# Kernel optimization log

Hardware: AMD Instinct MI355X
Metric: run time of the kernel (lower is better)

## Reference

```python
import jax, jax.numpy as jnp
import numpy as np

HS = 256      # hidden_size
HD = 256      # hidden_dim
B, L, S = 256, 400, 512
N = B * L
E = N * 4
NEG_SLOPE = 0.2


def setup_inputs() -> dict:
    key = jax.random.key(0)
    ks = iter(jax.random.split(key, 48))
    def rn(shape, scale=0.05):
        return jax.random.normal(next(ks), shape, jnp.float32) * scale
    inp = {}
    inp['emb'] = jax.random.normal(next(ks), (N, 640), jnp.float32)
    inp['x_tokens'] = jax.random.randint(next(ks), (N,), 0, 6, jnp.int32)
    inp['edge_src'] = jax.random.randint(next(ks), (E,), 0, N, jnp.int32)
    inp['edge_dst'] = jax.random.randint(next(ks), (E,), 0, N, jnp.int32)
    inp['batch_ids'] = (jnp.arange(N, dtype=jnp.int32) // L)
    inp['pos_ids'] = (jnp.arange(N, dtype=jnp.int32) % L)
    inp['mask'] = (jnp.arange(S)[None, :] < L).astype(jnp.float32) * jnp.ones((B, 1), jnp.float32)
    # parameters
    inp['emb_table'] = rn((6, HS))
    inp['W_e2g'] = rn((640, HS)); inp['b_e2g'] = jnp.zeros((HS,), jnp.float32)
    # GAT layers: (in, heads*out), att_src/att_dst [heads, out], bias [out]
    inp['W1'] = rn((HS, 4 * HD)); inp['asrc1'] = rn((4, HD)); inp['adst1'] = rn((4, HD)); inp['b1'] = jnp.zeros((HD,), jnp.float32)
    inp['W2'] = rn((HD, 4 * HD)); inp['asrc2'] = rn((4, HD)); inp['adst2'] = rn((4, HD)); inp['b2'] = jnp.zeros((HD,), jnp.float32)
    inp['W3'] = rn((HD, 1 * HS)); inp['asrc3'] = rn((1, HS)); inp['adst3'] = rn((1, HS)); inp['b3'] = jnp.zeros((HS,), jnp.float32)
    inp['W_le'] = rn((640, HS)); inp['b_le'] = jnp.zeros((HS,), jnp.float32)
    # CNN conv kernels: OIH layout [out=128, in=256, k]
    inp['k7'] = rn((HS // 2, HS, 7)); inp['cb7'] = jnp.zeros((HS // 2,), jnp.float32)
    inp['k11'] = rn((HS // 2, HS, 11)); inp['cb11'] = jnp.zeros((HS // 2,), jnp.float32)
    inp['k15'] = rn((HS // 2, HS, 15)); inp['cb15'] = jnp.zeros((HS // 2,), jnp.float32)
    inp['Wl1'] = rn((HS // 2, 512)); inp['bl1'] = jnp.zeros((512,), jnp.float32)
    inp['Wl2'] = rn((512, HS)); inp['bl2'] = jnp.zeros((HS,), jnp.float32)
    return inp


def _gat(x, src, dst, W, a_src, a_dst, b, heads, out_dim):
    # PyG GATConv, concat=False, eval (no dropout), with self-loops.
    n = x.shape[0]
    h = (x @ W).reshape(n, heads, out_dim)             # [N,H,C]
    al_s = (h * a_src[None]).sum(-1)                   # [N,H]
    al_d = (h * a_dst[None]).sum(-1)                   # [N,H]
    e = al_s[src] + al_d[dst]                          # [E,H]
    e = jnp.where(e > 0, e, NEG_SLOPE * e)             # leaky_relu(0.2)
    m = jax.ops.segment_max(e, dst, num_segments=n)
    m = jnp.where(jnp.isfinite(m), m, 0.0)
    ex = jnp.exp(e - m[dst])
    denom = jax.ops.segment_sum(ex, dst, num_segments=n) + 1e-16
    alpha = ex / denom[dst]                            # [E,H]
    out = jax.ops.segment_sum(alpha[:, :, None] * h[src], dst, num_segments=n)
    return out.mean(axis=1) + b                        # concat=False -> mean over heads


def _conv1d(x, w, b, pad):
    # x: [B,C,S], w: [O,I,k]
    y = jax.lax.conv_general_dilated(x, w, (1,), [(pad, pad)],
                                     dimension_numbers=('NCH', 'OIH', 'NCH'))
    return y + b[None, :, None]


def reference(emb, x_tokens, edge_src, edge_dst, batch_ids, pos_ids, mask,
              emb_table, W_e2g, b_e2g,
              W1, asrc1, adst1, b1, W2, asrc2, adst2, b2, W3, asrc3, adst3, b3,
              W_le, b_le, k7, cb7, k11, cb11, k15, cb15, Wl1, bl1, Wl2, bl2):
    n = emb.shape[0]
    # self-loops (PyG GATConv default)
    loops = jnp.arange(n, dtype=edge_src.dtype)
    src = jnp.concatenate([edge_src, loops])
    dst = jnp.concatenate([edge_dst, loops])

    x_r = emb_table[x_tokens]                          # [N,HS]
    x_g = jax.nn.relu(emb @ W_e2g + b_e2g)             # [N,HS]
    x = jax.nn.relu(_gat(x_g, src, dst, W1, asrc1, adst1, b1, 4, HD))
    x = jax.nn.relu(_gat(x, src, dst, W2, asrc2, adst2, b2, 4, HD))
    x = jax.nn.relu(_gat(x, src, dst, W3, asrc3, adst3, b3, 1, HS))

    emb_l = jax.nn.relu(emb @ W_le + b_le)             # [N,HS]

    # ragged -> padded [B,S,HS] via scatter (vectorized form of the python loop)
    zeros = jnp.zeros((mask.shape[0], S, HS), jnp.float32)
    out_r = zeros.at[batch_ids, pos_ids].set((x_r + emb_l) / 2)

    # CNN (eval: dropout = identity)
    xc = out_r.transpose(0, 2, 1)                      # [B,HS,S]
    x1 = _conv1d(xc, k7, cb7, 3)
    x2 = _conv1d(xc, k11, cb11, 5)
    x3 = _conv1d(xc, k15, cb15, 7)
    xc = ((x1 + x2 + x3) / 3).transpose(0, 2, 1)       # [B,S,128]
    xc = jax.nn.relu(xc @ Wl1 + bl1) @ Wl2 + bl2       # [B,S,HS]

    emb_seq = (xc * mask[:, :, None]).mean(axis=1)     # [B,HS]
    return emb_seq
```

## Files before the change

kernel.cpp:

```cpp
#include <hip/hip_runtime.h>

#define NNODES 102400
#define NBATCH 256
#define LSEQ   400
#define SPAD   416
#define HS     256
#define KDIM   640
#define OC     128
#define NTAP   15
#define H1     512
#define STILE  80
#define SROWS  94

typedef __attribute__((ext_vector_type(8))) short short8;
typedef __attribute__((ext_vector_type(4))) float floatx4;

__device__ inline unsigned short f2bf(float f) {
    unsigned u = __builtin_bit_cast(unsigned, f);
    unsigned r = (u + 0x7FFFu + ((u >> 16) & 1u)) >> 16;
    return (unsigned short)r;
}

__device__ inline void gld_lds16(const void* g, void* l) {
    __builtin_amdgcn_global_load_lds(
        (const __attribute__((address_space(1))) unsigned int*)g,
        (__attribute__((address_space(3))) unsigned int*)l, 16, 0, 0);
}

__global__ __launch_bounds__(256) void setup_all(
    const float* __restrict__ k7, const float* __restrict__ k11,
    const float* __restrict__ k15, const float* __restrict__ cb7,
    const float* __restrict__ cb11, const float* __restrict__ cb15,
    const float* __restrict__ W_le, const float* __restrict__ Wl1,
    unsigned short* __restrict__ Wpk, float* __restrict__ bc,
    unsigned short* __restrict__ Wle_pk, unsigned short* __restrict__ Wl1_pk,
    unsigned short* __restrict__ seq, float* __restrict__ A_acc)
{
    int bid = blockIdx.x, tid = threadIdx.x;
    if (bid < 512) {
        int idx = bid * 256 + tid;
        int b = idx >> 9, within = idx & 511;
        int rowi = within >> 5, c = within & 31;
        int srow = rowi < 8 ? rowi : 400 + rowi;
        ((uint4*)seq)[((size_t)b * SPAD + srow) * 32 + c] = make_uint4(0u, 0u, 0u, 0u);
    } else if (bid < 2432) {
        int idx = (bid - 512) * 256 + tid;
        int oc = idx & (OC - 1);
        int ic = (idx >> 7) & (HS - 1);
        int d  = idx / (OC * HS);
        float wv = k15[(oc * HS + ic) * 15 + d];
        int t11 = d - 2;
        if (t11 >= 0 && t11 < 11) wv += k11[(oc * HS + ic) * 11 + t11];
        int t7 = d - 4;
        if (t7 >= 0 && t7 < 7)   wv += k7[(oc * HS + ic) * 7 + t7];
        wv *= (1.0f / 3.0f);
        int kc = ic >> 6, ks = (ic >> 5) & 1, qq = (ic >> 3) & 3, j = ic & 7;
        int nt = oc >> 4, n = oc & 15;
        int pidx = ((((d * 4 + kc) * 2 + ks) * 8 + nt) * 64 + (qq * 16 + n)) * 8 + j;
        Wpk[pidx] = f2bf(wv);
        if (idx < OC) bc[idx] = (cb7[idx] + cb11[idx] + cb15[idx]) * (1.0f / 3.0f);
    } else if (bid < 3072) {
        int idx = (bid - 2432) * 256 + tid;
        int k = idx >> 8, col = idx & 255;
        int t = k >> 6, ks = (k >> 5) & 1, qq = (k >> 3) & 3, j = k & 7;
        int nt = col >> 4, n = col & 15;
        int pidx = (((t * 2 + ks) * 16 + nt) * 64 + (qq * 16 + n)) * 8 + j;
        Wle_pk[pidx] = f2bf(W_le[k * 256 + col]);
    } else if (bid < 3328) {
        int idx = (bid - 3072) * 256 + tid;
        int k = idx >> 9, col = idx & 511;
        int ks = k >> 5, qq = (k >> 3) & 3, j = k & 7;
        int jbb = col >> 7, nhnt = (col >> 4) & 7, n = col & 15;
        int pidx = jbb * 16384 + ((ks * 8 + nhnt) * 64 + (qq * 16 + n)) * 8 + j;
        Wl1_pk[pidx] = f2bf(Wl1[k * 512 + col]);
    } else {
        int idx = (bid - 3328) * 256 + tid;
        ((float4*)A_acc)[idx] = make_float4(0.f, 0.f, 0.f, 0.f);
    }
}

union GemmSm {
    struct { unsigned short As[64][72]; unsigned short Bsh[16384]; } s;
    unsigned short Cs[64][264];
};

__global__ __launch_bounds__(256) void gemm_emb(
    const float* __restrict__ emb, const int* __restrict__ x_tokens,
    const float* __restrict__ emb_table,
    const unsigned short* __restrict__ Wle_pk, const float* __restrict__ b_le,
    unsigned short* __restrict__ seq)
{
    __shared__ __align__(16) GemmSm g;
    int row0 = blockIdx.x * 64;
    int tid = threadIdx.x;
    int w = tid >> 6, lane = tid & 63;
    int q = lane >> 4, m = lane & 15;
    int mh = w >> 1, nh = w & 1;

    int ar = tid >> 2;
    int ac = (tid & 3) * 16;

    floatx4 acc[2][8] = {};
    const uint4* wp = (const uint4*)Wle_pk;

    for (int t = 0; t < 10; t++) {
        __syncthreads();
        {
            const float4* src = (const float4*)&emb[(size_t)(row0 + ar) * KDIM + t * 64 + ac];
            #pragma unroll
            for (int u = 0; u < 4; u++) {
                float4 f = src[u];
                ushort4 h;
                h.x = f2bf(f.x); h.y = f2bf(f.y); h.z = f2bf(f.z); h.w = f2bf(f.w);
                *(ushort4*)&g.s.As[ar][ac + u * 4] = h;
            }
        }
        #pragma unroll
        for (int i = 0; i < 8; i++) {
            gld_lds16(wp + (size_t)t * 2048 + i * 256 + tid,
                      &g.s.Bsh[(size_t)(i * 256 + w * 64) * 8]);
        }
        __syncthreads();

        #pragma unroll
        for (int ks = 0; ks < 2; ks++) {
            short8 a0 = *(const short8*)&g.s.As[mh * 32 + m][ks * 32 + q * 8];
            short8 a1 = *(const short8*)&g.s.As[mh * 32 + 16 + m][ks * 32 + q * 8];
            #pragma unroll
            for (int nt = 0; nt < 8; nt++) {
                short8 bf = *(const short8*)&g.s.Bsh[(size_t)((ks * 16 + nh * 8 + nt) * 64 + lane) * 8];
                acc[0][nt] = __builtin_amdgcn_mfma_f32_16x16x32_bf16(a0, bf, acc[0][nt], 0, 0, 0);
                acc[1][nt] = __builtin_amdgcn_mfma_f32_16x16x32_bf16(a1, bf, acc[1][nt], 0, 0, 0);
            }
        }
    }

    __syncthreads();
    #pragma unroll
    for (int nt = 0; nt < 8; nt++) {
        int col = nh * 128 + nt * 16 + m;
        float blv = b_le[col];
        #pragma unroll
        for (int mt = 0; mt < 2; mt++) {
            #pragma unroll
            for (int r = 0; r < 4; r++) {
                int row = mh * 32 + mt * 16 + q * 4 + r;
                int tok = x_tokens[row0 + row];
                float v = acc[mt][nt][r] + blv;
                v = v > 0.f ? v : 0.f;
                g.Cs[row][col] = f2bf(0.5f * (v + emb_table[tok * HS + col]));
            }
        }
    }
    __syncthreads();
    #pragma unroll
    for (int rr = 0; rr < 16; rr++) {
        int node = row0 + w * 16 + rr;
        int b = node / LSEQ;
        int p = node - b * LSEQ;
        ushort4 val = *(const ushort4*)&g.Cs[w * 16 + rr][lane * 4];
        *(ushort4*)&seq[((size_t)b * SPAD + (p + 8)) * HS + lane * 4] = val;
    }
}

union ConvSm {
    unsigned short As[SROWS][264];
    struct {
        union {
            float red[STILE * 132];
            unsigned short Bsh[16384];
        } rb;
        unsigned short abf[STILE][136];
    } p2;
};

__device__ __forceinline__ void conv_load_B(
    const short8* __restrict__ wb, int c, int kh, int nh, int lane, short8 bf[8])
{
    int d = c >> 1, kc = kh * 2 + (c & 1);
    const short8* bp = wb + (size_t)(d * 4 + kc) * 1024 + nh * 256 + lane;
    #pragma unroll
    for (int ks = 0; ks < 2; ks++)
        #pragma unroll
        for (int nt = 0; nt < 4; nt++)
            bf[ks * 4 + nt] = bp[(ks * 8 + nt) * 64];
}

__device__ __forceinline__ void conv_mfma_chunk(
    const unsigned short (*As)[264], floatx4 acc[5][4],
    const short8 bf[8], int c, int kh, int m, int q)
{
    int d = c >> 1, kc = kh * 2 + (c & 1);
    #pragma unroll
    for (int ks = 0; ks < 2; ks++) {
        #pragma unroll
        for (int mt = 0; mt < 5; mt++) {
            short8 a = *(const short8*)&As[mt * 16 + m + d][kc * 64 + ks * 32 + q * 8];
            #pragma unroll
            for (int nt = 0; nt < 4; nt++)
                acc[mt][nt] = __builtin_amdgcn_mfma_f32_16x16x32_bf16(a, bf[ks * 4 + nt], acc[mt][nt], 0, 0, 0);
        }
    }
}

__global__ __launch_bounds__(256, 2) void conv_fused(
    const unsigned short* __restrict__ seq, const unsigned short* __restrict__ Wpk,
    const float* __restrict__ bc, const unsigned short* __restrict__ Wl1_pk,
    const float* __restrict__ bl1, float* __restrict__ A_acc)
{
    __shared__ __align__(16) ConvSm sm;

    int b  = blockIdx.y;
    int s0 = blockIdx.x * STILE;
    int tid = threadIdx.x;
    int w = tid >> 6, lane = tid & 63;
    int q = lane >> 4, m = lane & 15;
    int nh = w >> 1, kh = w & 1;

    const short8* wb = (const short8*)Wpk;
    short8 bufA[8], bufB[8];
    conv_load_B(wb, 0, kh, nh, lane, bufA);

    {
        const uint4* sp = (const uint4*)(seq + ((size_t)b * SPAD + s0 + 1) * HS);
        #pragma unroll
        for (int pass = 0; pass < 12; pass++) {
            int idx = pass * 256 + tid;
            if (idx < SROWS * 32) {
                int r = idx >> 5, c = idx & 31;
                *(uint4*)&sm.As[r][c * 8] = sp[r * 32 + c];
            }
        }
    }
    __syncthreads();

    floatx4 acc[5][4] = {};

    for (int c = 0; c < 30; c += 2) {
        conv_load_B(wb, c + 1, kh, nh, lane, bufB);
        conv_mfma_chunk(sm.As, acc, bufA, c, kh, m, q);
        if (c + 2 < 30) conv_load_B(wb, c + 2, kh, nh, lane, bufA);
        conv_mfma_chunk(sm.As, acc, bufB, c + 1, kh, m, q);
    }

    __syncthreads();
    if (kh == 1) {
        #pragma unroll
        for (int mt = 0; mt < 5; mt++)
            #pragma unroll
            for (int nt = 0; nt < 4; nt++)
                #pragma unroll
                for (int r = 0; r < 4; r++)
                    sm.p2.rb.red[(mt * 16 + q * 4 + r) * 132 + nh * 64 + nt * 16 + m] = acc[mt][nt][r];
    }
    __syncthreads();
    if (kh == 0) {
        #pragma unroll
        for (int mt = 0; mt < 5; mt++)
            #pragma unroll
            for (int nt = 0; nt < 4; nt++)
                #pragma unroll
                for (int r = 0; r < 4; r++)
                    sm.p2.rb.red[(mt * 16 + q * 4 + r) * 132 + nh * 64 + nt * 16 + m] += acc[mt][nt][r];
    }
    __syncthreads();
    {
        float b0 = bc[lane * 2], b1 = bc[lane * 2 + 1];
        #pragma unroll
        for (int rr = 0; rr < 20; rr++) {
            int row = w * 20 + rr;
            float2 v = *(const float2*)&sm.p2.rb.red[row * 132 + lane * 2];
            unsigned uo = (unsigned)f2bf(v.x + b0) | ((unsigned)f2bf(v.y + b1) << 16);
            *(unsigned*)&sm.p2.abf[row][lane * 2] = uo;
        }
    }
    __syncthreads();

    for (int jb = 0; jb < 4; jb++) {
        {
            const uint4* wp = (const uint4*)(Wl1_pk + (size_t)jb * 16384);
            #pragma unroll
            for (int i = 0; i < 8; i++)
                gld_lds16(wp + i * 256 + tid, &sm.p2.rb.Bsh[(size_t)(i * 256 + w * 64) * 8]);
        }
        __syncthreads();

        floatx4 acc2[5][2] = {};
        #pragma unroll
        for (int ks = 0; ks < 4; ks++) {
            short8 bf0 = *(const short8*)&sm.p2.rb.Bsh[(size_t)((ks * 8 + w * 2 + 0) * 64 + lane) * 8];
            short8 bf1 = *(const short8*)&sm.p2.rb.Bsh[(size_t)((ks * 8 + w * 2 + 1) * 64 + lane) * 8];
            #pragma unroll
            for (int mt = 0; mt < 5; mt++) {
                short8 a = *(const short8*)&sm.p2.abf[mt * 16 + m][ks * 32 + q * 8];
                acc2[mt][0] = __builtin_amdgcn_mfma_f32_16x16x32_bf16(a, bf0, acc2[mt][0], 0, 0, 0);
                acc2[mt][1] = __builtin_amdgcn_mfma_f32_16x16x32_bf16(a, bf1, acc2[mt][1], 0, 0, 0);
            }
        }
        #pragma unroll
        for (int nt = 0; nt < 2; nt++) {
            int j = jb * 128 + w * 32 + nt * 16 + m;
            float blv = bl1[j];
            float vsum = 0.f;
            #pragma unroll
            for (int mt = 0; mt < 5; mt++)
                #pragma unroll
                for (int r = 0; r < 4; r++) {
                    float v = acc2[mt][nt][r] + blv;
                    vsum += v > 0.f ? v : 0.f;
                }
            vsum += __shfl_xor(vsum, 16, 64);
            vsum += __shfl_xor(vsum, 32, 64);
            if (q == 0) atomicAdd(&A_acc[(size_t)b * H1 + j], vsum);
        }
        __syncthreads();
    }
}

__global__ __launch_bounds__(256) void final_out(
    const float* __restrict__ A_acc, const float* __restrict__ Wl2,
    const float* __restrict__ bl2, float* __restrict__ out)
{
    __shared__ float a[H1];
    int b = blockIdx.x, tid = threadIdx.x;
    a[tid] = A_acc[(size_t)b * H1 + tid];
    a[tid + 256] = A_acc[(size_t)b * H1 + tid + 256];
    __syncthreads();
    float acc = 0.f;
    #pragma unroll 8
    for (int k = 0; k < H1; k++)
        acc += a[k] * Wl2[(size_t)k * HS + tid];
    out[(size_t)b * HS + tid] = acc * (1.0f / 512.0f) + bl2[tid] * (400.0f / 512.0f);
}

extern "C" void kernel_launch(void* const* d_in, const int* in_sizes, int n_in,
                              void* d_out, int out_size, void* d_ws, size_t ws_size,
                              hipStream_t stream)
{
    const float* emb       = (const float*)d_in[0];
    const int*   x_tokens  = (const int*)d_in[1];
    const float* emb_table = (const float*)d_in[7];
    const float* W_le = (const float*)d_in[22];
    const float* b_le = (const float*)d_in[23];
    const float* k7   = (const float*)d_in[24];
    const float* cb7  = (const float*)d_in[25];
    const float* k11  = (const float*)d_in[26];
    const float* cb11 = (const float*)d_in[27];
    const float* k15  = (const float*)d_in[28];
    const float* cb15 = (const float*)d_in[29];
    const float* Wl1  = (const float*)d_in[30];
    const float* bl1  = (const float*)d_in[31];
    const float* Wl2  = (const float*)d_in[32];
    const float* bl2  = (const float*)d_in[33];
    float* out = (float*)d_out;

    char* p = (char*)d_ws;
    unsigned short* seqb = (unsigned short*)p;       p += (size_t)NBATCH * SPAD * HS * 2;
    unsigned short* Wpk = (unsigned short*)p;        p += (size_t)NTAP * HS * OC * 2;
    unsigned short* Wle_pk = (unsigned short*)p;     p += (size_t)KDIM * HS * 2;
    unsigned short* Wl1_pk = (unsigned short*)p;     p += (size_t)OC * H1 * 2;
    float* bcv = (float*)p;                          p += 512;
    float* A_acc = (float*)p;                        p += (size_t)NBATCH * H1 * 4;

    setup_all<<<dim3(3456), 256, 0, stream>>>(
        k7, k11, k15, cb7, cb11, cb15, W_le, Wl1,
        Wpk, bcv, Wle_pk, Wl1_pk, seqb, A_acc);
    gemm_emb<<<dim3(NNODES / 64), 256, 0, stream>>>(
        emb, x_tokens, emb_table, Wle_pk, b_le, seqb);
    conv_fused<<<dim3(5, NBATCH), 256, 0, stream>>>(
        seqb, Wpk, bcv, Wl1_pk, bl1, A_acc);
    final_out<<<NBATCH, 256, 0, stream>>>(A_acc, Wl2, bl2, out);
}
```

Before: 592.6 us.

## Enlarge GEMM row tile and cut conv LDS/register use for higher occupancy

The embedding GEMM now processes 128 rows per block instead of 64, so each Wle tile staged in LDS is reused across twice as many rows. The epilogue writes in two halves to keep the Cs buffer the same size. In the conv kernel, B fragments are prefetched in half-chunks (4 instead of 8 short8 registers) and the split-K reduction goes through a 40-row buffer in two passes. Wl1 fragments are read directly into registers instead of being staged in LDS, which removes a per-iteration barrier. Together these shrink LDS and register use so launch bounds can ask for 3 blocks per CU, at the cost of extra barriers and more global reads of Wl1 per wave.

Result: slower. 638.2 us (+7.7%).

```diff
diff --git a/kernel.cpp b/kernel.cpp
--- a/kernel.cpp
+++ b/kernel.cpp
@@ -80,7 +80,7 @@
 }
 
 union GemmSm {
-    struct { unsigned short As[64][72]; unsigned short Bsh[16384]; } s;
+    struct { unsigned short As[128][72]; unsigned short Bsh[16384]; } s;
     unsigned short Cs[64][264];
 };
 
@@ -91,16 +91,16 @@
     unsigned short* __restrict__ seq)
 {
     __shared__ __align__(16) GemmSm g;
-    int row0 = blockIdx.x * 64;
+    int row0 = blockIdx.x * 128;
     int tid = threadIdx.x;
     int w = tid >> 6, lane = tid & 63;
     int q = lane >> 4, m = lane & 15;
     int mh = w >> 1, nh = w & 1;
 
-    int ar = tid >> 2;
-    int ac = (tid & 3) * 16;
-
-    floatx4 acc[2][8] = {};
+    int ar = tid >> 1;
+    int ac = (tid & 1) * 32;
+
+    floatx4 acc[4][8] = {};
     const uint4* wp = (const uint4*)Wle_pk;
 
     for (int t = 0; t < 10; t++) {
@@ -108,7 +108,7 @@
         {
             const float4* src = (const float4*)&emb[(size_t)(row0 + ar) * KDIM + t * 64 + ac];
             #pragma unroll
-            for (int u = 0; u < 4; u++) {
+            for (int u = 0; u < 8; u++) {
                 float4 f = src[u];
                 ushort4 h;
                 h.x = f2bf(f.x); h.y = f2bf(f.y); h.z = f2bf(f.z); h.w = f2bf(f.w);
@@ -124,86 +124,88 @@
 
         #pragma unroll
         for (int ks = 0; ks < 2; ks++) {
-            short8 a0 = *(const short8*)&g.s.As[mh * 32 + m][ks * 32 + q * 8];
-            short8 a1 = *(const short8*)&g.s.As[mh * 32 + 16 + m][ks * 32 + q * 8];
+            short8 a0 = *(const short8*)&g.s.As[mh * 64 +  0 + m][ks * 32 + q * 8];
+            short8 a1 = *(const short8*)&g.s.As[mh * 64 + 16 + m][ks * 32 + q * 8];
+            short8 a2 = *(const short8*)&g.s.As[mh * 64 + 32 + m][ks * 32 + q * 8];
+            short8 a3 = *(const short8*)&g.s.As[mh * 64 + 48 + m][ks * 32 + q * 8];
             #pragma unroll
             for (int nt = 0; nt < 8; nt++) {
                 short8 bf = *(const short8*)&g.s.Bsh[(size_t)((ks * 16 + nh * 8 + nt) * 64 + lane) * 8];
                 acc[0][nt] = __builtin_amdgcn_mfma_f32_16x16x32_bf16(a0, bf, acc[0][nt], 0, 0, 0);
                 acc[1][nt] = __builtin_amdgcn_mfma_f32_16x16x32_bf16(a1, bf, acc[1][nt], 0, 0, 0);
-            }
-        }
-    }
-
-    __syncthreads();
-    #pragma unroll
-    for (int nt = 0; nt < 8; nt++) {
-        int col = nh * 128 + nt * 16 + m;
-        float blv = b_le[col];
-        #pragma unroll
-        for (int mt = 0; mt < 2; mt++) {
-            #pragma unroll
-            for (int r = 0; r < 4; r++) {
-                int row = mh * 32 + mt * 16 + q * 4 + r;
-                int tok = x_tokens[row0 + row];
-                float v = acc[mt][nt][r] + blv;
-                v = v > 0.f ? v : 0.f;
-                g.Cs[row][col] = f2bf(0.5f * (v + emb_table[tok * HS + col]));
-            }
-        }
-    }
-    __syncthreads();
-    #pragma unroll
-    for (int rr = 0; rr < 16; rr++) {
-        int node = row0 + w * 16 + rr;
-        int b = node / LSEQ;
-        int p = node - b * LSEQ;
-        ushort4 val = *(const ushort4*)&g.Cs[w * 16 + rr][lane * 4];
-        *(ushort4*)&seq[((size_t)b * SPAD + (p + 8)) * HS + lane * 4] = val;
+                acc[2][nt] = __builtin_amdgcn_mfma_f32_16x16x32_bf16(a2, bf, acc[2][nt], 0, 0, 0);
+                acc[3][nt] = __builtin_amdgcn_mfma_f32_16x16x32_bf16(a3, bf, acc[3][nt], 0, 0, 0);
+            }
+        }
+    }
+
+    #pragma unroll
+    for (int h = 0; h < 2; h++) {
+        __syncthreads();
+        if (mh == h) {
+            #pragma unroll
+            for (int mt = 0; mt < 4; mt++) {
+                #pragma unroll
+                for (int r = 0; r < 4; r++) {
+                    int lrow = mt * 16 + q * 4 + r;
+                    int tokb = x_tokens[row0 + h * 64 + lrow] * HS;
+                    #pragma unroll
+                    for (int nt = 0; nt < 8; nt++) {
+                        int col = nh * 128 + nt * 16 + m;
+                        float v = acc[mt][nt][r] + b_le[col];
+                        v = v > 0.f ? v : 0.f;
+                        g.Cs[lrow][col] = f2bf(0.5f * (v + emb_table[tokb + col]));
+                    }
+                }
+            }
+        }
+        __syncthreads();
+        #pragma unroll
+        for (int rr = 0; rr < 16; rr++) {
+            int node = row0 + h * 64 + w * 16 + rr;
+            int b = node / LSEQ;
+            int p = node - b * LSEQ;
+            ushort4 val = *(const ushort4*)&g.Cs[w * 16 + rr][lane * 4];
+            *(ushort4*)&seq[((size_t)b * SPAD + (p + 8)) * HS + lane * 4] = val;
+        }
     }
 }
 
 union ConvSm {
     unsigned short As[SROWS][264];
     struct {
-        union {
-            float red[STILE * 132];
-            unsigned short Bsh[16384];
-        } rb;
+        float red[40 * 132];
         unsigned short abf[STILE][136];
     } p2;
 };
 
-__device__ __forceinline__ void conv_load_B(
-    const short8* __restrict__ wb, int c, int kh, int nh, int lane, short8 bf[8])
-{
+__device__ __forceinline__ void conv_load_Bh(
+    const short8* __restrict__ wb, int h, int kh, int nh, int lane, short8 bf[4])
+{
+    int c = h >> 1, ks = h & 1;
     int d = c >> 1, kc = kh * 2 + (c & 1);
-    const short8* bp = wb + (size_t)(d * 4 + kc) * 1024 + nh * 256 + lane;
-    #pragma unroll
-    for (int ks = 0; ks < 2; ks++)
+    const short8* bp = wb + (size_t)(d * 4 + kc) * 1024 + nh * 256 + ks * 512 + lane;
+    #pragma unroll
+    for (int nt = 0; nt < 4; nt++)
+        bf[nt] = bp[nt * 64];
+}
+
+__device__ __forceinline__ void conv_mfma_half(
+    const unsigned short (*As)[264], floatx4 acc[5][4],
+    const short8 bf[4], int h, int kh, int m, int q)
+{
+    int c = h >> 1, ks = h & 1;
+    int d = c >> 1, kc = kh * 2 + (c & 1);
+    #pragma unroll
+    for (int mt = 0; mt < 5; mt++) {
+        short8 a = *(const short8*)&As[mt * 16 + m + d][kc * 64 + ks * 32 + q * 8];
         #pragma unroll
         for (int nt = 0; nt < 4; nt++)
-            bf[ks * 4 + nt] = bp[(ks * 8 + nt) * 64];
-}
-
-__device__ __forceinline__ void conv_mfma_chunk(
-    const unsigned short (*As)[264], floatx4 acc[5][4],
-    const short8 bf[8], int c, int kh, int m, int q)
-{
-    int d = c >> 1, kc = kh * 2 + (c & 1);
-    #pragma unroll
-    for (int ks = 0; ks < 2; ks++) {
-        #pragma unroll
-        for (int mt = 0; mt < 5; mt++) {
-            short8 a = *(const short8*)&As[mt * 16 + m + d][kc * 64 + ks * 32 + q * 8];
-            #pragma unroll
-            for (int nt = 0; nt < 4; nt++)
-                acc[mt][nt] = __builtin_amdgcn_mfma_f32_16x16x32_bf16(a, bf[ks * 4 + nt], acc[mt][nt], 0, 0, 0);
-        }
-    }
-}
-
-__global__ __launch_bounds__(256, 2) void conv_fused(
+            acc[mt][nt] = __builtin_amdgcn_mfma_f32_16x16x32_bf16(a, bf[nt], acc[mt][nt], 0, 0, 0);
+    }
+}
+
+__global__ __launch_bounds__(256, 3) void conv_fused(
     const unsigned short* __restrict__ seq, const unsigned short* __restrict__ Wpk,
     const float* __restrict__ bc, const unsigned short* __restrict__ Wl1_pk,
     const float* __restrict__ bl1, float* __restrict__ A_acc)
@@ -218,8 +220,8 @@
     int nh = w >> 1, kh = w & 1;
 
     const short8* wb = (const short8*)Wpk;
-    short8 bufA[8], bufB[8];
-    conv_load_B(wb, 0, kh, nh, lane, bufA);
+    short8 bA[4], bB[4];
+    conv_load_Bh(wb, 0, kh, nh, lane, bA);
 
     {
         const uint4* sp = (const uint4*)(seq + ((size_t)b * SPAD + s0 + 1) * HS);
@@ -236,66 +238,88 @@
 
     floatx4 acc[5][4] = {};
 
-    for (int c = 0; c < 30; c += 2) {
-        conv_load_B(wb, c + 1, kh, nh, lane, bufB);
-        conv_mfma_chunk(sm.As, acc, bufA, c, kh, m, q);
-        if (c + 2 < 30) conv_load_B(wb, c + 2, kh, nh, lane, bufA);
-        conv_mfma_chunk(sm.As, acc, bufB, c + 1, kh, m, q);
-    }
-
+    for (int h = 0; h < 60; h += 2) {
+        conv_load_Bh(wb, h + 1, kh, nh, lane, bB);
+        conv_mfma_half(sm.As, acc, bA, h, kh, m, q);
+        if (h + 2 < 60) conv_load_Bh(wb, h + 2, kh, nh, lane, bA);
+        conv_mfma_half(sm.As, acc, bB, h + 1, kh, m, q);
+    }
+
+    float bc0 = bc[lane * 2], bc1 = bc[lane * 2 + 1];
     __syncthreads();
-    if (kh == 1) {
-        #pragma unroll
-        for (int mt = 0; mt < 5; mt++)
-            #pragma unroll
-            for (int nt = 0; nt < 4; nt++)
-                #pragma unroll
-                for (int r = 0; r < 4; r++)
-                    sm.p2.rb.red[(mt * 16 + q * 4 + r) * 132 + nh * 64 + nt * 16 + m] = acc[mt][nt][r];
-    }
-    __syncthreads();
-    if (kh == 0) {
-        #pragma unroll
-        for (int mt = 0; mt < 5; mt++)
-            #pragma unroll
-            for (int nt = 0; nt < 4; nt++)
-                #pragma unroll
-                for (int r = 0; r < 4; r++)
-                    sm.p2.rb.red[(mt * 16 + q * 4 + r) * 132 + nh * 64 + nt * 16 + m] += acc[mt][nt][r];
-    }
-    __syncthreads();
-    {
-        float b0 = bc[lane * 2], b1 = bc[lane * 2 + 1];
-        #pragma unroll
-        for (int rr = 0; rr < 20; rr++) {
-            int row = w * 20 + rr;
-            float2 v = *(const float2*)&sm.p2.rb.red[row * 132 + lane * 2];
-            unsigned uo = (unsigned)f2bf(v.x + b0) | ((unsigned)f2bf(v.y + b1) << 16);
-            *(unsigned*)&sm.p2.abf[row][lane * 2] = uo;
-        }
-    }
-    __syncthreads();
-
+    #pragma unroll
+    for (int hh = 0; hh < 2; hh++) {
+        if (kh == 1) {
+            #pragma unroll
+            for (int mt = 0; mt < 5; mt++)
+                #pragma unroll
+                for (int nt = 0; nt < 4; nt++)
+                    #pragma unroll
+                    for (int r = 0; r < 4; r++) {
+                        int row = mt * 16 + q * 4 + r;
+                        if (row >= hh * 40 && row < hh * 40 + 40)
+                            sm.p2.red[(row - hh * 40) * 132 + nh * 64 + nt * 16 + m] = acc[mt][nt][r];
+                    }
+        }
+        __syncthreads();
+        if (kh == 0) {
+            #pragma unroll
+            for (int mt = 0; mt < 5; mt++)
+                #pragma unroll
+                for (int nt = 0; nt < 4; nt++)
+                    #pragma unroll
+                    for (int r = 0; r < 4; r++) {
+                        int row = mt * 16 + q * 4 + r;
+                        if (row >= hh * 40 && row < hh * 40 + 40)
+                            sm.p2.red[(row - hh * 40) * 132 + nh * 64 + nt * 16 + m] += acc[mt][nt][r];
+                    }
+        }
+        __syncthreads();
+        #pragma unroll
+        for (int rr = 0; rr < 10; rr++) {
+            int lrow = w * 10 + rr;
+            float2 v = *(const float2*)&sm.p2.red[lrow * 132 + lane * 2];
+            unsigned uo = (unsigned)f2bf(v.x + bc0) | ((unsigned)f2bf(v.y + bc1) << 16);
+            *(unsigned*)&sm.p2.abf[hh * 40 + lrow][lane * 2] = uo;
+        }
+        __syncthreads();
+    }
+
+    const short8* wl1 = (const short8*)Wl1_pk;
+    short8 f0[8], f1[8];
+    #pragma unroll
+    for (int ks = 0; ks < 4; ks++)
+        #pragma unroll
+        for (int nt = 0; nt < 2; nt++)
+            f0[ks * 2 + nt] = wl1[(ks * 8 + w * 2 + nt) * 64 + lane];
+    #pragma unroll
+    for (int ks = 0; ks < 4; ks++)
+        #pragma unroll
+        for (int nt = 0; nt < 2; nt++)
+            f1[ks * 2 + nt] = wl1[2048 + (ks * 8 + w * 2 + nt) * 64 + lane];
+
+    #pragma unroll
     for (int jb = 0; jb < 4; jb++) {
-        {
-            const uint4* wp = (const uint4*)(Wl1_pk + (size_t)jb * 16384);
-            #pragma unroll
-            for (int i = 0; i < 8; i++)
-                gld_lds16(wp + i * 256 + tid, &sm.p2.rb.Bsh[(size_t)(i * 256 + w * 64) * 8]);
-        }
-        __syncthreads();
-
         floatx4 acc2[5][2] = {};
+        const short8* fcur = (jb & 1) ? f1 : f0;
         #pragma unroll
         for (int ks = 0; ks < 4; ks++) {
-            short8 bf0 = *(const short8*)&sm.p2.rb.Bsh[(size_t)((ks * 8 + w * 2 + 0) * 64 + lane) * 8];
-            short8 bf1 = *(const short8*)&sm.p2.rb.Bsh[(size_t)((ks * 8 + w * 2 + 1) * 64 + lane) * 8];
+            short8 bf0 = fcur[ks * 2 + 0];
+            short8 bf1 = fcur[ks * 2 + 1];
             #pragma unroll
             for (int mt = 0; mt < 5; mt++) {
                 short8 a = *(const short8*)&sm.p2.abf[mt * 16 + m][ks * 32 + q * 8];
                 acc2[mt][0] = __builtin_amdgcn_mfma_f32_16x16x32_bf16(a, bf0, acc2[mt][0], 0, 0, 0);
                 acc2[mt][1] = __builtin_amdgcn_mfma_f32_16x16x32_bf16(a, bf1, acc2[mt][1], 0, 0, 0);
             }
+        }
+        if (jb < 2) {
+            short8* fnext = (jb & 1) ? f1 : f0;
+            #pragma unroll
+            for (int ks = 0; ks < 4; ks++)
+                #pragma unroll
+                for (int nt = 0; nt < 2; nt++)
+                    fnext[ks * 2 + nt] = wl1[(size_t)(jb + 2) * 2048 + (ks * 8 + w * 2 + nt) * 64 + lane];
         }
         #pragma unroll
         for (int nt = 0; nt < 2; nt++) {
@@ -313,7 +337,6 @@
             vsum += __shfl_xor(vsum, 32, 64);
             if (q == 0) atomicAdd(&A_acc[(size_t)b * H1 + j], vsum);
         }
-        __syncthreads();
     }
 }
 
@@ -365,7 +388,7 @@
     setup_all<<<dim3(3456), 256, 0, stream>>>(
         k7, k11, k15, cb7, cb11, cb15, W_le, Wl1,
         Wpk, bcv, Wle_pk, Wl1_pk, seqb, A_acc);
-    gemm_emb<<<dim3(NNODES / 64), 256, 0, stream>>>(
+    gemm_emb<<<dim3(NNODES / 128), 256, 0, stream>>>(
         emb, x_tokens, emb_table, Wle_pk, b_le, seqb);
     conv_fused<<<dim3(5, NBATCH), 256, 0, stream>>>(
         seqb, Wpk, bcv, Wl1_pk, bl1, A_acc);
```
